# Optimization experiments

Hardware: AMD Instinct MI355X
Metric: run time of the kernel (lower is better)

## Reference

```python
import jax, jax.numpy as jnp
import numpy as np

N, DIN, DOUT = 8192, 512, 256


def setup_inputs() -> dict:
    key = jax.random.key(0)
    ks = jax.random.split(key, 8)
    s_in = 1.0 / np.sqrt(DIN)   # ~ torch Linear default init scale
    s_out = 1.0 / np.sqrt(DOUT)
    return {
        "x": jax.random.normal(ks[0], (N, DIN), jnp.float32),
        "Wm": jax.random.normal(ks[1], (DIN, DOUT), jnp.float32) * s_in,
        "Wn": jax.random.normal(ks[2], (DIN, DOUT), jnp.float32) * s_in,
        "Wr": jax.random.normal(ks[3], (DIN, DOUT), jnp.float32) * s_in,
        "Wt": jax.random.normal(ks[4], (DIN, DOUT), jnp.float32) * s_in,
        "Wrg": jax.random.normal(ks[5], (DOUT, DOUT), jnp.float32) * s_out,
        "brg": jnp.zeros((DOUT,), jnp.float32),
        "Wlg": jax.random.normal(ks[6], (DOUT, DOUT), jnp.float32) * s_out,
        "blg": jnp.zeros((DOUT,), jnp.float32),
        "Wp": jax.random.normal(ks[7], (DOUT, 1), jnp.float32) * s_out,
        "bp": jnp.zeros((1,), jnp.float32),
    }


def reference(x, Wm, Wn, Wr, Wt, Wrg, brg, Wlg, blg, Wp, bp):
    n = x.shape[0]
    xm = x @ Wm                      # [N, 256]
    xn = x @ Wn                      # [N, 256]
    # pairwise Euclidean distance via GEMM trick (avoids O(N^2*D) diff tensor)
    sq = (jnp.sum(xm * xm, axis=-1)[:, None]
          + jnp.sum(xn * xn, axis=-1)[None, :]
          - 2.0 * (xm @ xn.T))       # [N, N]
    dist = jnp.sqrt(jnp.maximum(sq, 0.0)) * 0.5
    exps = jnp.exp(-dist) / (n / 64.0)
    eye = jnp.eye(n, dtype=x.dtype)
    adj = exps * (1.0 - eye) + eye   # unit diagonal, scaled off-diagonal
    xr = adj @ (x @ Wr)              # graph conv: [N,N]@[N,256]
    xl = x @ Wt
    w = jax.nn.sigmoid(xr @ Wrg + brg + xl @ Wlg + blg)
    feat = (1.0 - w) * xr + w * xl   # gated fusion
    score = feat @ Wp + bp           # [N, 1]
    return adj, score
```

## Files before the change

### kernel.cpp

```cpp
#include <hip/hip_runtime.h>
#include <stdint.h>

typedef __attribute__((ext_vector_type(8))) short bf16x8;
typedef __attribute__((ext_vector_type(4))) float f32x4;
typedef __attribute__((ext_vector_type(4))) unsigned int u32x4;

__device__ __forceinline__ unsigned short f2bf(float f){
  unsigned u = __float_as_uint(f);
  u += 0x7FFFu + ((u >> 16) & 1u);
  return (unsigned short)(u >> 16);
}
__device__ __forceinline__ float bf2f(unsigned short s){
  return __uint_as_float(((unsigned)s) << 16);
}

__device__ __forceinline__ int lds_off(int r, int b){
  return r * 128 + (b ^ ((r & 7) << 4));
}
__device__ __forceinline__ int ldsP_off(int r, int b){
  return r * 256 + (b ^ ((r & 7) << 4));
}

__device__ __forceinline__ void cp16(const unsigned short* g, unsigned short* l){
  __builtin_amdgcn_global_load_lds(
      (const __attribute__((address_space(1))) unsigned int*)g,
      (__attribute__((address_space(3))) unsigned int*)l, 16, 0, 0);
}

template<int ROWS, int NT>
__device__ __forceinline__ void stage_async(unsigned short* lds, const unsigned short* g,
                                            long row0, long stride, long k0, int tid){
#pragma unroll
  for (int c = tid; c < ROWS * 8; c += NT){
    int r = c >> 3, s = c & 7;
    int ss = s ^ (r & 7);
    cp16(g + (row0 + r) * stride + k0 + ss * 8, lds + (long)(c & ~63) * 8);
  }
}

__device__ __forceinline__ int xcd_swz(int bid, int nwg){
  int q = nwg >> 3;
  return (bid & 7) * q + (bid >> 3);
}

__global__ __launch_bounds__(256) void k_prep(const float* x, const float* Wm, const float* Wn,
    const float* Wr, const float* Wt, const float* Wrg, const float* Wlg, const float* bp,
    unsigned short* WT, unsigned short* WcatT, unsigned short* xbf, float* nm, float* nn,
    float* score){
  long id = (long)blockIdx.x * 256 + threadIdx.x;
  if (id < 1024L * 512){
    int n = (int)(id >> 9), k = (int)(id & 511);
    const float* W = (n < 256) ? Wm : ((n < 512) ? Wn : ((n < 768) ? Wr : Wt));
    WT[id] = f2bf(W[(long)k * 256 + (n & 255)]);
  }
  if (id < 256L * 512){
    int n = (int)(id >> 9), k = (int)(id & 511);
    WcatT[id] = f2bf(k < 256 ? Wrg[(long)k * 256 + n] : Wlg[(long)(k - 256) * 256 + n]);
  }
  if (id < 8192){ score[id] = bp[0]; nm[id] = 0.f; nn[id] = 0.f; }
  long xe = id * 8;
  float4 v0 = *(const float4*)(x + xe);
  float4 v1 = *(const float4*)(x + xe + 4);
  unsigned short t[8] = { f2bf(v0.x), f2bf(v0.y), f2bf(v0.z), f2bf(v0.w),
                          f2bf(v1.x), f2bf(v1.y), f2bf(v1.z), f2bf(v1.w) };
  *(uint4*)(xbf + xe) = *(const uint4*)t;
}

__global__ __launch_bounds__(256, 3) void k_gemmA(const unsigned short* xbf, const unsigned short* WT,
    unsigned short* xm, unsigned short* xn, unsigned short* xwrT, unsigned short* xl,
    float* nm, float* nn){
  __shared__ unsigned short ldsA[128 * 64];
  __shared__ unsigned short ldsB[128 * 64];
  int tid = threadIdx.x, lane = tid & 63, w = tid >> 6;
  int r = lane & 15, gq = lane >> 4;
  int wi = w >> 1, wc = w & 1;
  int swz = xcd_swz(blockIdx.x, 512);
  int bm = swz & 63, bn = swz >> 6;

  f32x4 acc[4][4];
  f32x4 zero = {0.f, 0.f, 0.f, 0.f};
#pragma unroll
  for (int m = 0; m < 4; ++m)
#pragma unroll
    for (int n = 0; n < 4; ++n) acc[m][n] = zero;

  for (int k0 = 0; k0 < 512; k0 += 64){
    __syncthreads();
    stage_async<128, 256>(ldsA, xbf, (long)bm * 128, 512, k0, tid);
    stage_async<128, 256>(ldsB, WT, (long)bn * 128, 512, k0, tid);
    __syncthreads();
#pragma unroll
    for (int ks = 0; ks < 2; ++ks){
      int bb = ks * 64 + gq * 16;
      bf16x8 a[4], b[4];
#pragma unroll
      for (int m = 0; m < 4; ++m)
        a[m] = *(const bf16x8*)((const char*)ldsA + lds_off(wi * 64 + m * 16 + r, bb));
#pragma unroll
      for (int n = 0; n < 4; ++n)
        b[n] = *(const bf16x8*)((const char*)ldsB + lds_off(wc * 64 + n * 16 + r, bb));
#pragma unroll
      for (int m = 0; m < 4; ++m)
#pragma unroll
        for (int n = 0; n < 4; ++n)
          acc[m][n] = __builtin_amdgcn_mfma_f32_16x16x32_bf16(b[n], a[m], acc[m][n], 0, 0, 0);
    }
  }
#pragma unroll
  for (int m = 0; m < 4; ++m){
    int i = bm * 128 + wi * 64 + m * 16 + r;
#pragma unroll
    for (int n = 0; n < 4; ++n){
      int ng = bn * 128 + wc * 64 + n * 16 + gq * 4;
      int sector = ng >> 8, nc = ng & 255;
      unsigned short p[4] = { f2bf(acc[m][n][0]), f2bf(acc[m][n][1]),
                              f2bf(acc[m][n][2]), f2bf(acc[m][n][3]) };
      if (sector == 2){
#pragma unroll
        for (int q = 0; q < 4; ++q) xwrT[(long)(nc + q) * 8192 + i] = p[q];
      } else {
        unsigned short* dst = sector == 0 ? xm : (sector == 1 ? xn : xl);
        *(uint2*)(dst + (long)i * 256 + nc) = *(const uint2*)p;
      }
    }
    if (bn < 4){
      float s = 0.f;
#pragma unroll
      for (int n = 0; n < 4; ++n)
#pragma unroll
        for (int q = 0; q < 4; ++q) s += acc[m][n][q] * acc[m][n][q];
      s += __shfl_xor(s, 16);
      s += __shfl_xor(s, 32);
      if (gq == 0) atomicAdd(((bn < 2) ? nm : nn) + i, s);
    }
  }
}

__global__ __launch_bounds__(256, 2) void k_adj(const unsigned short* xm, const unsigned short* xn,
    const float* nm, const float* nn, float* adj, unsigned short* adjbf){
  __shared__ char smem[65536];
  char* ldsP = smem;

  int tid = threadIdx.x, lane = tid & 63, w = tid >> 6;
  int r = lane & 15, gq = lane >> 4;
  int wi = w >> 1, wj = w & 1;
  int swz = xcd_swz(blockIdx.x, 4096);
  int bm = swz & 63, bn = swz >> 6;

  f32x4 acc1[4][4];
  f32x4 zero = {0.f, 0.f, 0.f, 0.f};
#pragma unroll
  for (int m = 0; m < 4; ++m)
#pragma unroll
    for (int n = 0; n < 4; ++n) acc1[m][n] = zero;

  stage_async<128, 256>((unsigned short*)smem, xm, (long)bm * 128, 256, 0, tid);
  stage_async<128, 256>((unsigned short*)(smem + 16384), xn, (long)bn * 128, 256, 0, tid);
  __syncthreads();

#pragma unroll
  for (int t = 0; t < 4; ++t){
    char* cbuf = smem + (t & 1) * 32768;
    if (t < 3){
      char* nbuf = smem + ((t + 1) & 1) * 32768;
      stage_async<128, 256>((unsigned short*)nbuf, xm, (long)bm * 128, 256, (t + 1) * 64, tid);
      stage_async<128, 256>((unsigned short*)(nbuf + 16384), xn, (long)bn * 128, 256, (t + 1) * 64, tid);
    }
    unsigned short* ldsA = (unsigned short*)cbuf;
    unsigned short* ldsB = (unsigned short*)(cbuf + 16384);
    __builtin_amdgcn_s_setprio(1);
#pragma unroll
    for (int ks = 0; ks < 2; ++ks){
      int bb = ks * 64 + gq * 16;
      bf16x8 a[4], b[4];
#pragma unroll
      for (int m = 0; m < 4; ++m)
        a[m] = *(const bf16x8*)((const char*)ldsA + lds_off(wi * 64 + m * 16 + r, bb));
#pragma unroll
      for (int n = 0; n < 4; ++n)
        b[n] = *(const bf16x8*)((const char*)ldsB + lds_off(wj * 64 + n * 16 + r, bb));
#pragma unroll
      for (int m = 0; m < 4; ++m)
#pragma unroll
        for (int n = 0; n < 4; ++n)
          acc1[m][n] = __builtin_amdgcn_mfma_f32_16x16x32_bf16(b[n], a[m], acc1[m][n], 0, 0, 0);
    }
    __builtin_amdgcn_s_setprio(0);
    __syncthreads();
  }

  float nmi[4];
#pragma unroll
  for (int m = 0; m < 4; ++m) nmi[m] = nm[bm * 128 + wi * 64 + m * 16 + r];
#pragma unroll
  for (int n = 0; n < 4; ++n){
    int jl0 = wj * 64 + n * 16 + gq * 4;
    int jb = bn * 128 + jl0;
    float4 nn4 = *(const float4*)(nn + jb);
    const float nnq[4] = { nn4.x, nn4.y, nn4.z, nn4.w };
#pragma unroll
    for (int m = 0; m < 4; ++m){
      int il = wi * 64 + m * 16 + r;
      int i = bm * 128 + il;
      unsigned short pv[4];
#pragma unroll
      for (int q = 0; q < 4; ++q){
        float sq = nmi[m] + nnq[q] - 2.f * acc1[m][n][q];
        float d = sqrtf(fmaxf(sq, 0.f)) * 0.5f;
        float v = (i == jb + q) ? 1.f : __expf(-d) * (1.f / 128.f);
        pv[q] = f2bf(v);
      }
      *(uint2*)(ldsP + ldsP_off(il, jl0 * 2)) = *(const uint2*)pv;
    }
  }
  __syncthreads();

#pragma unroll
  for (int o = 0; o < 8; ++o){
    int c = o * 256 + tid;
    int row = c >> 4, cs = c & 15;
    unsigned short pb[8];
    *(uint4*)pb = *(const uint4*)(ldsP + ldsP_off(row, cs * 16));
    long ge = (long)(bm * 128 + row) * 8192 + bn * 128 + cs * 8;
    __builtin_nontemporal_store(*(const u32x4*)pb, (u32x4*)(adjbf + ge));
    f32x4 v0 = { bf2f(pb[0]), bf2f(pb[1]), bf2f(pb[2]), bf2f(pb[3]) };
    f32x4 v1 = { bf2f(pb[4]), bf2f(pb[5]), bf2f(pb[6]), bf2f(pb[7]) };
    __builtin_nontemporal_store(v0, (f32x4*)(adj + ge));
    __builtin_nontemporal_store(v1, (f32x4*)(adj + ge + 4));
  }
}

__global__ __launch_bounds__(512, 1) void k_xr(const unsigned short* adjbf,
    const unsigned short* xwrT, float* partial, int klen, int NS){
  __shared__ char smem[98304];
  int tid = threadIdx.x, lane = tid & 63, w = tid >> 6;
  int r = lane & 15, gq = lane >> 4;
  int wi = w >> 2, wc = w & 3;
  int sp = blockIdx.x % NS;
  int bm = blockIdx.x / NS;
  long j0 = (long)sp * klen;
  int nt = klen >> 6;

  f32x4 acc[4][4];
  f32x4 zero = {0.f, 0.f, 0.f, 0.f};
#pragma unroll
  for (int m = 0; m < 4; ++m)
#pragma unroll
    for (int n = 0; n < 4; ++n) acc[m][n] = zero;

  stage_async<128, 512>((unsigned short*)smem, adjbf, (long)bm * 128, 8192, j0, tid);
  stage_async<256, 512>((unsigned short*)(smem + 16384), xwrT, 0, 8192, j0, tid);
  __syncthreads();

  for (int t = 0; t < nt; ++t){
    char* cbuf = smem + (t & 1) * 49152;
    if (t + 1 < nt){
      char* nbuf = smem + ((t + 1) & 1) * 49152;
      long jn = j0 + (long)(t + 1) * 64;
      stage_async<128, 512>((unsigned short*)nbuf, adjbf, (long)bm * 128, 8192, jn, tid);
      stage_async<256, 512>((unsigned short*)(nbuf + 16384), xwrT, 0, 8192, jn, tid);
    }
    unsigned short* ldsA = (unsigned short*)cbuf;
    unsigned short* ldsB = (unsigned short*)(cbuf + 16384);
    __builtin_amdgcn_s_setprio(1);
#pragma unroll
    for (int ks = 0; ks < 2; ++ks){
      int bb = ks * 64 + gq * 16;
      bf16x8 a[4], b[4];
#pragma unroll
      for (int m = 0; m < 4; ++m)
        a[m] = *(const bf16x8*)((const char*)ldsA + lds_off(wi * 64 + m * 16 + r, bb));
#pragma unroll
      for (int n = 0; n < 4; ++n)
        b[n] = *(const bf16x8*)((const char*)ldsB + lds_off(wc * 64 + n * 16 + r, bb));
#pragma unroll
      for (int m = 0; m < 4; ++m)
#pragma unroll
        for (int n = 0; n < 4; ++n)
          acc[m][n] = __builtin_amdgcn_mfma_f32_16x16x32_bf16(b[n], a[m], acc[m][n], 0, 0, 0);
    }
    __builtin_amdgcn_s_setprio(0);
    __syncthreads();
  }

  float* dst = partial + (long)sp * 8192 * 256;
#pragma unroll
  for (int m = 0; m < 4; ++m){
    int i = bm * 128 + wi * 64 + m * 16 + r;
#pragma unroll
    for (int n = 0; n < 4; ++n){
      int cb = wc * 64 + n * 16 + gq * 4;
      __builtin_nontemporal_store(acc[m][n], (f32x4*)(dst + (long)i * 256 + cb));
    }
  }
}

__global__ __launch_bounds__(512, 2) void k_gate(const float* partial, int S,
    const unsigned short* xl, const unsigned short* WcatT,
    const float* brg, const float* blg, const float* Wp, float* score){
  __shared__ unsigned short ldsA[128 * 64];
  __shared__ unsigned short ldsB[256 * 64];
  int tid = threadIdx.x, lane = tid & 63, w = tid >> 6;
  int r = lane & 15, gq = lane >> 4;
  int wi = w >> 2, wc = w & 3;
  int bm = blockIdx.x;

  f32x4 acc[4][4];
  f32x4 zero = {0.f, 0.f, 0.f, 0.f};
#pragma unroll
  for (int m = 0; m < 4; ++m)
#pragma unroll
    for (int n = 0; n < 4; ++n) acc[m][n] = zero;

  uint2 xrf[4][4], xlf[4][4];

  for (int t = 0; t < 8; ++t){
    __syncthreads();
    if (t < 4){
#pragma unroll
      for (int u = 0; u < 2; ++u){
        int c = tid + u * 512;
        int rr = c >> 3, s = c & 7;
        long gi = (long)(bm * 128 + rr) * 256 + t * 64 + s * 8;
        f32x4 a0 = __builtin_nontemporal_load((const f32x4*)(partial + gi));
        f32x4 a1 = __builtin_nontemporal_load((const f32x4*)(partial + gi + 4));
        for (int sp = 1; sp < S; ++sp){
          long go = (long)sp * 8192 * 256 + gi;
          a0 += __builtin_nontemporal_load((const f32x4*)(partial + go));
          a1 += __builtin_nontemporal_load((const f32x4*)(partial + go + 4));
        }
        unsigned short tb[8] = { f2bf(a0[0]), f2bf(a0[1]), f2bf(a0[2]), f2bf(a0[3]),
                                 f2bf(a1[0]), f2bf(a1[1]), f2bf(a1[2]), f2bf(a1[3]) };
        *(uint4*)((char*)ldsA + lds_off(rr, s * 16)) = *(const uint4*)tb;
      }
    } else {
      stage_async<128, 512>(ldsA, xl, (long)bm * 128, 256, (t - 4) * 64, tid);
    }
    stage_async<256, 512>(ldsB, WcatT, 0, 512, (long)t * 64, tid);
    __syncthreads();

    if (t == wc || t == wc + 4){
#pragma unroll
      for (int m = 0; m < 4; ++m){
        int il = wi * 64 + m * 16 + r;
#pragma unroll
        for (int n = 0; n < 4; ++n){
          uint2 v = *(const uint2*)((const char*)ldsA + lds_off(il, (n * 16 + gq * 4) * 2));
          if (t < 4) xrf[m][n] = v; else xlf[m][n] = v;
        }
      }
    }
#pragma unroll
    for (int ks = 0; ks < 2; ++ks){
      int bb = ks * 64 + gq * 16;
      bf16x8 a[4], b[4];
#pragma unroll
      for (int m = 0; m < 4; ++m)
        a[m] = *(const bf16x8*)((const char*)ldsA + lds_off(wi * 64 + m * 16 + r, bb));
#pragma unroll
      for (int n = 0; n < 4; ++n)
        b[n] = *(const bf16x8*)((const char*)ldsB + lds_off(wc * 64 + n * 16 + r, bb));
#pragma unroll
      for (int m = 0; m < 4; ++m)
#pragma unroll
        for (int n = 0; n < 4; ++n)
          acc[m][n] = __builtin_amdgcn_mfma_f32_16x16x32_bf16(b[n], a[m], acc[m][n], 0, 0, 0);
    }
  }

#pragma unroll
  for (int m = 0; m < 4; ++m){
    int i = bm * 128 + wi * 64 + m * 16 + r;
    float part = 0.f;
#pragma unroll
    for (int n = 0; n < 4; ++n){
      int cb = wc * 64 + n * 16 + gq * 4;
      float4 b4  = *(const float4*)(brg + cb);
      float4 l4  = *(const float4*)(blg + cb);
      float4 wp4 = *(const float4*)(Wp + cb);
      const unsigned short* xr4 = (const unsigned short*)&xrf[m][n];
      const unsigned short* xl4 = (const unsigned short*)&xlf[m][n];
      const float bq[4] = { b4.x, b4.y, b4.z, b4.w };
      const float lq[4] = { l4.x, l4.y, l4.z, l4.w };
      const float pq[4] = { wp4.x, wp4.y, wp4.z, wp4.w };
#pragma unroll
      for (int q = 0; q < 4; ++q){
        float arg = acc[m][n][q] + bq[q] + lq[q];
        float wv = 1.f / (1.f + __expf(-arg));
        float feat = (1.f - wv) * bf2f(xr4[q]) + wv * bf2f(xl4[q]);
        part += feat * pq[q];
      }
    }
    part += __shfl_xor(part, 16);
    part += __shfl_xor(part, 32);
    if (gq == 0) atomicAdd(score + i, part);
  }
}

extern "C" void kernel_launch(void* const* d_in, const int* in_sizes, int n_in,
                              void* d_out, int out_size, void* d_ws, size_t ws_size,
                              hipStream_t stream){
  const float* x   = (const float*)d_in[0];
  const float* Wm  = (const float*)d_in[1];
  const float* Wn  = (const float*)d_in[2];
  const float* Wr  = (const float*)d_in[3];
  const float* Wt  = (const float*)d_in[4];
  const float* Wrg = (const float*)d_in[5];
  const float* brg = (const float*)d_in[6];
  const float* Wlg = (const float*)d_in[7];
  const float* blg = (const float*)d_in[8];
  const float* Wp  = (const float*)d_in[9];
  const float* bp  = (const float*)d_in[10];

  float* adj   = (float*)d_out;
  float* score = adj + 8192L * 8192;

  char* wsb = (char*)d_ws;
  unsigned short* xm    = (unsigned short*)(wsb);
  unsigned short* xn    = (unsigned short*)(wsb + (4L  << 20));
  unsigned short* xwrT  = (unsigned short*)(wsb + (8L  << 20));
  unsigned short* xl    = (unsigned short*)(wsb + (12L << 20));
  float*          nm    = (float*)         (wsb + (20L << 20));
  float*          nn    = nm + 8192;
  unsigned short* WT    = (unsigned short*)(wsb + (21L << 20));
  unsigned short* WcatT = (unsigned short*)(wsb + (22L << 20));
  unsigned short* xbf   = (unsigned short*)(wsb + (23L << 20));
  unsigned short* adjbf = (unsigned short*)(wsb + (31L << 20));
  float*          partial = (float*)(wsb + (159L << 20));

  size_t base = 159L << 20;
  int NS = 1;
  if      (ws_size >= base + 4 * (8L << 20)) NS = 4;
  else if (ws_size >= base + 2 * (8L << 20)) NS = 2;

  k_prep  <<<2048, 256, 0, stream>>>(x, Wm, Wn, Wr, Wt, Wrg, Wlg, bp, WT, WcatT, xbf, nm, nn, score);
  k_gemmA <<<512, 256, 0, stream>>>(xbf, WT, xm, xn, xwrT, xl, nm, nn);
  k_adj   <<<4096, 256, 0, stream>>>(xm, xn, nm, nn, adj, adjbf);
  k_xr    <<<64 * NS, 512, 0, stream>>>(adjbf, xwrT, partial, 8192 / NS, NS);
  k_gate  <<<64, 512, 0, stream>>>(partial, NS, xl, WcatT, brg, blg, Wp, score);
}
```

Baseline: 294.7 us.

## Fuse adjacency generation with adj@xWr GEMM to drop bf16 adj round trip

Merges the adjacency kernel and the graph-conv GEMM into one kernel. Each block owns a 128-row strip and a split of column tiles: it computes the distance tile, writes the exp tile as bf16 into LDS, and multiplies it directly with xWr. This removes the 128 MB bf16 adj write and its re-read. The fp32 adj store of each tile is deferred and interleaved with the next tile's first GEMM. The grid shrinks to 64*NS blocks (up to 512 with NS=8), which risks low parallelism on 256 CUs. The xWr staging is also no longer double-buffered.

New measurement: 287.9 us. -2.3%, faster.

```diff
diff --git a/kernel.cpp b/kernel.cpp
--- a/kernel.cpp
+++ b/kernel.cpp
@@ -136,152 +136,145 @@
   }
 }
 
-__global__ __launch_bounds__(256, 2) void k_adj(const unsigned short* xm, const unsigned short* xn,
-    const float* nm, const float* nn, float* adj, unsigned short* adjbf){
-  __shared__ char smem[65536];
-  char* ldsP = smem;
+__global__ __launch_bounds__(512, 1) void k_fused(
+    const unsigned short* xm, const unsigned short* xn,
+    const float* nm, const float* nn, const unsigned short* xwrT,
+    float* adj, float* partial, int ntiles, int NS){
+  __shared__ char smem[131072];
+  char* ldsP = smem + 65536;
+  unsigned short* ldsW = (unsigned short*)(smem + 98304);
 
   int tid = threadIdx.x, lane = tid & 63, w = tid >> 6;
   int r = lane & 15, gq = lane >> 4;
-  int wi = w >> 1, wj = w & 1;
-  int swz = xcd_swz(blockIdx.x, 4096);
-  int bm = swz & 63, bn = swz >> 6;
-
-  f32x4 acc1[4][4];
+  int wi = w >> 2, wj = w & 3;
+  int sp = blockIdx.x % NS, bm = blockIdx.x / NS;
+
   f32x4 zero = {0.f, 0.f, 0.f, 0.f};
+  f32x4 acc2[4][4];
 #pragma unroll
   for (int m = 0; m < 4; ++m)
 #pragma unroll
-    for (int n = 0; n < 4; ++n) acc1[m][n] = zero;
-
-  stage_async<128, 256>((unsigned short*)smem, xm, (long)bm * 128, 256, 0, tid);
-  stage_async<128, 256>((unsigned short*)(smem + 16384), xn, (long)bn * 128, 256, 0, tid);
-  __syncthreads();
-
-#pragma unroll
-  for (int t = 0; t < 4; ++t){
-    char* cbuf = smem + (t & 1) * 32768;
-    if (t < 3){
-      char* nbuf = smem + ((t + 1) & 1) * 32768;
-      stage_async<128, 256>((unsigned short*)nbuf, xm, (long)bm * 128, 256, (t + 1) * 64, tid);
-      stage_async<128, 256>((unsigned short*)(nbuf + 16384), xn, (long)bn * 128, 256, (t + 1) * 64, tid);
-    }
-    unsigned short* ldsA = (unsigned short*)cbuf;
-    unsigned short* ldsB = (unsigned short*)(cbuf + 16384);
-    __builtin_amdgcn_s_setprio(1);
-#pragma unroll
-    for (int ks = 0; ks < 2; ++ks){
-      int bb = ks * 64 + gq * 16;
-      bf16x8 a[4], b[4];
-#pragma unroll
-      for (int m = 0; m < 4; ++m)
-        a[m] = *(const bf16x8*)((const char*)ldsA + lds_off(wi * 64 + m * 16 + r, bb));
-#pragma unroll
-      for (int n = 0; n < 4; ++n)
-        b[n] = *(const bf16x8*)((const char*)ldsB + lds_off(wj * 64 + n * 16 + r, bb));
-#pragma unroll
-      for (int m = 0; m < 4; ++m)
+    for (int n = 0; n < 4; ++n) acc2[m][n] = zero;
+
+  float nmi[4];
+#pragma unroll
+  for (int m = 0; m < 4; ++m) nmi[m] = nm[bm * 128 + wi * 64 + m * 16 + r];
+
+  long prevColBase = 0;
+
+  for (int t = 0; t < ntiles; ++t){
+    int bn = sp * ntiles + t;
+    f32x4 acc1[4][2];
+#pragma unroll
+    for (int m = 0; m < 4; ++m)
+#pragma unroll
+      for (int n = 0; n < 2; ++n) acc1[m][n] = zero;
+
+    stage_async<128, 512>((unsigned short*)smem, xm, (long)bm * 128, 256, 0, tid);
+    stage_async<128, 512>((unsigned short*)(smem + 16384), xn, (long)bn * 128, 256, 0, tid);
+    __syncthreads();
+#pragma unroll
+    for (int kk = 0; kk < 4; ++kk){
+      char* cb = smem + (kk & 1) * 32768;
+      if (kk < 3){
+        char* nb = smem + ((kk + 1) & 1) * 32768;
+        stage_async<128, 512>((unsigned short*)nb, xm, (long)bm * 128, 256, (kk + 1) * 64, tid);
+        stage_async<128, 512>((unsigned short*)(nb + 16384), xn, (long)bn * 128, 256, (kk + 1) * 64, tid);
+      }
+      if (t > 0){
+        int row = kk * 32 + (tid >> 4), cs = tid & 15;
+        uint4 pv = *(const uint4*)(ldsP + ldsP_off(row, cs * 16));
+        const unsigned short* pb = (const unsigned short*)&pv;
+        long ge = (long)(bm * 128 + row) * 8192 + prevColBase + cs * 8;
+        f32x4 v0 = { bf2f(pb[0]), bf2f(pb[1]), bf2f(pb[2]), bf2f(pb[3]) };
+        f32x4 v1 = { bf2f(pb[4]), bf2f(pb[5]), bf2f(pb[6]), bf2f(pb[7]) };
+        __builtin_nontemporal_store(v0, (f32x4*)(adj + ge));
+        __builtin_nontemporal_store(v1, (f32x4*)(adj + ge + 4));
+      }
+      unsigned short* ldsA = (unsigned short*)cb;
+      unsigned short* ldsB = (unsigned short*)(cb + 16384);
+      __builtin_amdgcn_s_setprio(1);
+#pragma unroll
+      for (int ks = 0; ks < 2; ++ks){
+        int bb = ks * 64 + gq * 16;
+        bf16x8 a[4], b[2];
+#pragma unroll
+        for (int m = 0; m < 4; ++m)
+          a[m] = *(const bf16x8*)((const char*)ldsA + lds_off(wi * 64 + m * 16 + r, bb));
+#pragma unroll
+        for (int n = 0; n < 2; ++n)
+          b[n] = *(const bf16x8*)((const char*)ldsB + lds_off(wj * 32 + n * 16 + r, bb));
+#pragma unroll
+        for (int m = 0; m < 4; ++m)
+#pragma unroll
+          for (int n = 0; n < 2; ++n)
+            acc1[m][n] = __builtin_amdgcn_mfma_f32_16x16x32_bf16(b[n], a[m], acc1[m][n], 0, 0, 0);
+      }
+      __builtin_amdgcn_s_setprio(0);
+      __syncthreads();
+    }
+
+#pragma unroll
+    for (int n = 0; n < 2; ++n){
+      int jl0 = wj * 32 + n * 16 + gq * 4;
+      int jb = bn * 128 + jl0;
+      float4 nn4 = *(const float4*)(nn + jb);
+      const float nnq[4] = { nn4.x, nn4.y, nn4.z, nn4.w };
+#pragma unroll
+      for (int m = 0; m < 4; ++m){
+        int il = wi * 64 + m * 16 + r;
+        int i = bm * 128 + il;
+        unsigned short pv[4];
+#pragma unroll
+        for (int q = 0; q < 4; ++q){
+          float sq = nmi[m] + nnq[q] - 2.f * acc1[m][n][q];
+          float d = sqrtf(fmaxf(sq, 0.f)) * 0.5f;
+          float v = (i == jb + q) ? 1.f : __expf(-d) * (1.f / 128.f);
+          pv[q] = f2bf(v);
+        }
+        *(uint2*)(ldsP + ldsP_off(il, jl0 * 2)) = *(const uint2*)pv;
+      }
+    }
+    __syncthreads();
+
+#pragma unroll
+    for (int kh = 0; kh < 2; ++kh){
+      stage_async<256, 512>(ldsW, xwrT, 0, 8192, (long)bn * 128 + kh * 64, tid);
+      __syncthreads();
+      __builtin_amdgcn_s_setprio(1);
+#pragma unroll
+      for (int ks = 0; ks < 2; ++ks){
+        bf16x8 a[4], b[4];
+#pragma unroll
+        for (int m = 0; m < 4; ++m)
+          a[m] = *(const bf16x8*)(ldsP + ldsP_off(wi * 64 + m * 16 + r, kh * 128 + ks * 64 + gq * 16));
 #pragma unroll
         for (int n = 0; n < 4; ++n)
-          acc1[m][n] = __builtin_amdgcn_mfma_f32_16x16x32_bf16(b[n], a[m], acc1[m][n], 0, 0, 0);
-    }
-    __builtin_amdgcn_s_setprio(0);
-    __syncthreads();
-  }
-
-  float nmi[4];
-#pragma unroll
-  for (int m = 0; m < 4; ++m) nmi[m] = nm[bm * 128 + wi * 64 + m * 16 + r];
-#pragma unroll
-  for (int n = 0; n < 4; ++n){
-    int jl0 = wj * 64 + n * 16 + gq * 4;
-    int jb = bn * 128 + jl0;
-    float4 nn4 = *(const float4*)(nn + jb);
-    const float nnq[4] = { nn4.x, nn4.y, nn4.z, nn4.w };
-#pragma unroll
-    for (int m = 0; m < 4; ++m){
-      int il = wi * 64 + m * 16 + r;
-      int i = bm * 128 + il;
-      unsigned short pv[4];
-#pragma unroll
-      for (int q = 0; q < 4; ++q){
-        float sq = nmi[m] + nnq[q] - 2.f * acc1[m][n][q];
-        float d = sqrtf(fmaxf(sq, 0.f)) * 0.5f;
-        float v = (i == jb + q) ? 1.f : __expf(-d) * (1.f / 128.f);
-        pv[q] = f2bf(v);
-      }
-      *(uint2*)(ldsP + ldsP_off(il, jl0 * 2)) = *(const uint2*)pv;
-    }
-  }
-  __syncthreads();
-
-#pragma unroll
-  for (int o = 0; o < 8; ++o){
-    int c = o * 256 + tid;
+          b[n] = *(const bf16x8*)((const char*)ldsW + lds_off(wj * 64 + n * 16 + r, ks * 64 + gq * 16));
+#pragma unroll
+        for (int m = 0; m < 4; ++m)
+#pragma unroll
+          for (int n = 0; n < 4; ++n)
+            acc2[m][n] = __builtin_amdgcn_mfma_f32_16x16x32_bf16(b[n], a[m], acc2[m][n], 0, 0, 0);
+      }
+      __builtin_amdgcn_s_setprio(0);
+      __syncthreads();
+    }
+    prevColBase = (long)bn * 128;
+  }
+
+#pragma unroll
+  for (int o = 0; o < 4; ++o){
+    int c = o * 512 + tid;
     int row = c >> 4, cs = c & 15;
-    unsigned short pb[8];
-    *(uint4*)pb = *(const uint4*)(ldsP + ldsP_off(row, cs * 16));
-    long ge = (long)(bm * 128 + row) * 8192 + bn * 128 + cs * 8;
-    __builtin_nontemporal_store(*(const u32x4*)pb, (u32x4*)(adjbf + ge));
+    uint4 pv = *(const uint4*)(ldsP + ldsP_off(row, cs * 16));
+    const unsigned short* pb = (const unsigned short*)&pv;
+    long ge = (long)(bm * 128 + row) * 8192 + prevColBase + cs * 8;
     f32x4 v0 = { bf2f(pb[0]), bf2f(pb[1]), bf2f(pb[2]), bf2f(pb[3]) };
     f32x4 v1 = { bf2f(pb[4]), bf2f(pb[5]), bf2f(pb[6]), bf2f(pb[7]) };
     __builtin_nontemporal_store(v0, (f32x4*)(adj + ge));
     __builtin_nontemporal_store(v1, (f32x4*)(adj + ge + 4));
   }
-}
-
-__global__ __launch_bounds__(512, 1) void k_xr(const unsigned short* adjbf,
-    const unsigned short* xwrT, float* partial, int klen, int NS){
-  __shared__ char smem[98304];
-  int tid = threadIdx.x, lane = tid & 63, w = tid >> 6;
-  int r = lane & 15, gq = lane >> 4;
-  int wi = w >> 2, wc = w & 3;
-  int sp = blockIdx.x % NS;
-  int bm = blockIdx.x / NS;
-  long j0 = (long)sp * klen;
-  int nt = klen >> 6;
-
-  f32x4 acc[4][4];
-  f32x4 zero = {0.f, 0.f, 0.f, 0.f};
-#pragma unroll
-  for (int m = 0; m < 4; ++m)
-#pragma unroll
-    for (int n = 0; n < 4; ++n) acc[m][n] = zero;
-
-  stage_async<128, 512>((unsigned short*)smem, adjbf, (long)bm * 128, 8192, j0, tid);
-  stage_async<256, 512>((unsigned short*)(smem + 16384), xwrT, 0, 8192, j0, tid);
-  __syncthreads();
-
-  for (int t = 0; t < nt; ++t){
-    char* cbuf = smem + (t & 1) * 49152;
-    if (t + 1 < nt){
-      char* nbuf = smem + ((t + 1) & 1) * 49152;
-      long jn = j0 + (long)(t + 1) * 64;
-      stage_async<128, 512>((unsigned short*)nbuf, adjbf, (long)bm * 128, 8192, jn, tid);
-      stage_async<256, 512>((unsigned short*)(nbuf + 16384), xwrT, 0, 8192, jn, tid);
-    }
-    unsigned short* ldsA = (unsigned short*)cbuf;
-    unsigned short* ldsB = (unsigned short*)(cbuf + 16384);
-    __builtin_amdgcn_s_setprio(1);
-#pragma unroll
-    for (int ks = 0; ks < 2; ++ks){
-      int bb = ks * 64 + gq * 16;
-      bf16x8 a[4], b[4];
-#pragma unroll
-      for (int m = 0; m < 4; ++m)
-        a[m] = *(const bf16x8*)((const char*)ldsA + lds_off(wi * 64 + m * 16 + r, bb));
-#pragma unroll
-      for (int n = 0; n < 4; ++n)
-        b[n] = *(const bf16x8*)((const char*)ldsB + lds_off(wc * 64 + n * 16 + r, bb));
-#pragma unroll
-      for (int m = 0; m < 4; ++m)
-#pragma unroll
-        for (int n = 0; n < 4; ++n)
-          acc[m][n] = __builtin_amdgcn_mfma_f32_16x16x32_bf16(b[n], a[m], acc[m][n], 0, 0, 0);
-    }
-    __builtin_amdgcn_s_setprio(0);
-    __syncthreads();
-  }
 
   float* dst = partial + (long)sp * 8192 * 256;
 #pragma unroll
@@ -289,8 +282,8 @@
     int i = bm * 128 + wi * 64 + m * 16 + r;
 #pragma unroll
     for (int n = 0; n < 4; ++n){
-      int cb = wc * 64 + n * 16 + gq * 4;
-      __builtin_nontemporal_store(acc[m][n], (f32x4*)(dst + (long)i * 256 + cb));
+      int cb = wj * 64 + n * 16 + gq * 4;
+      __builtin_nontemporal_store(acc2[m][n], (f32x4*)(dst + (long)i * 256 + cb));
     }
   }
 }
@@ -425,17 +418,16 @@
   unsigned short* WT    = (unsigned short*)(wsb + (21L << 20));
   unsigned short* WcatT = (unsigned short*)(wsb + (22L << 20));
   unsigned short* xbf   = (unsigned short*)(wsb + (23L << 20));
-  unsigned short* adjbf = (unsigned short*)(wsb + (31L << 20));
-  float*          partial = (float*)(wsb + (159L << 20));
-
-  size_t base = 159L << 20;
+  float*          partial = (float*)(wsb + (31L << 20));
+
+  size_t base = 31L << 20;
   int NS = 1;
-  if      (ws_size >= base + 4 * (8L << 20)) NS = 4;
+  if      (ws_size >= base + 8 * (8L << 20)) NS = 8;
+  else if (ws_size >= base + 4 * (8L << 20)) NS = 4;
   else if (ws_size >= base + 2 * (8L << 20)) NS = 2;
 
   k_prep  <<<2048, 256, 0, stream>>>(x, Wm, Wn, Wr, Wt, Wrg, Wlg, bp, WT, WcatT, xbf, nm, nn, score);
   k_gemmA <<<512, 256, 0, stream>>>(xbf, WT, xm, xn, xwrT, xl, nm, nn);
-  k_adj   <<<4096, 256, 0, stream>>>(xm, xn, nm, nn, adj, adjbf);
-  k_xr    <<<64 * NS, 512, 0, stream>>>(adjbf, xwrT, partial, 8192 / NS, NS);
+  k_fused <<<64 * NS, 512, 0, stream>>>(xm, xn, nm, nn, xwrT, adj, partial, 64 / NS, NS);
   k_gate  <<<64, 512, 0, stream>>>(partial, NS, xl, WcatT, brg, blg, Wp, score);
 }
```
